# Kernel tuning notes

Measured on AMD Instinct MI355X. Metric: run time of the kernel, lower is better.

## Reference

```python
import jax, jax.numpy as jnp
import numpy as np

B, IN, H = 8192, 1024, 1024


def setup_inputs() -> dict:
    key = jax.random.key(0)
    kx, kh, kc, kwx, kwh = jax.random.split(key, 5)
    return {
        "x": jax.random.normal(kx, (B, IN), dtype=jnp.float32),
        "h": jax.random.normal(kh, (B, H), dtype=jnp.float32),
        "c": jax.random.normal(kc, (B, H), dtype=jnp.float32),
        # 8 Dense layers fused: gate order [i, f, g, o] along last axis
        "Wx": jax.random.normal(kwx, (IN, 4 * H), dtype=jnp.float32) * 0.02,
        "Wh": jax.random.normal(kwh, (H, 4 * H), dtype=jnp.float32) * 0.02,
        "bx": jnp.zeros((4 * H,), dtype=jnp.float32),
        "bh": jnp.zeros((4 * H,), dtype=jnp.float32),
    }


def reference(x, h, c, Wx, Wh, bx, bh):
    # Fused equivalent of the 8 separate Dense layers:
    #   gate_k = x @ Wx[:, k] + bx[k] + h @ Wh[:, k] + bh[k]
    gates = x @ Wx + h @ Wh + (bx + bh)  # [B, 4H]
    i, f, g, o = jnp.split(gates, 4, axis=-1)
    i = jax.nn.sigmoid(i)
    f = jax.nn.sigmoid(f)
    g = jnp.tanh(g)
    o = jax.nn.sigmoid(o)
    c_new = f * c + i * g
    h_new = o * jnp.tanh(c_new)
    # Original returns (out_gate, hidden_state, cell_state)
    return (o, h_new, c_new)
```

## Files before the change

### kernel.cpp

```cpp
#include <hip/hip_runtime.h>
#include <hip/hip_bf16.h>

typedef __attribute__((ext_vector_type(8))) short bf16x8;
typedef __attribute__((ext_vector_type(4))) float f32x4;
typedef __attribute__((ext_vector_type(4))) unsigned short u16x4;
typedef __attribute__((ext_vector_type(8))) unsigned short u16x8;

#define B_DIM 8192
#define H_DIM 1024
#define K_DIM 2048
#define N_DIM 4096
#define BH (B_DIM * H_DIM)

__device__ __forceinline__ unsigned short f2bf(float f) {
    union { float f; unsigned u; } v; v.f = f;
    unsigned r = v.u + 0x7FFFu + ((v.u >> 16) & 1u);
    return (unsigned short)(r >> 16);
}

__device__ __forceinline__ void gload16(const void* g, void* l) {
    __builtin_amdgcn_global_load_lds(
        (const __attribute__((address_space(1))) void*)g,
        (__attribute__((address_space(3))) void*)l, 16, 0, 0);
}

__global__ void build_a(const float* __restrict__ x, const float* __restrict__ h,
                        unsigned short* __restrict__ Abf) {
    int gid = blockIdx.x * 256 + threadIdx.x;
    int m   = gid >> 9;
    int rem = gid & 511;
    int p   = rem >> 8;
    int k4  = rem & 255;
    const float* src = (p ? h : x) + m * 1024 + k4 * 4;
    float4 v = *(const float4*)src;
    u16x4 o = { f2bf(v.x), f2bf(v.y), f2bf(v.z), f2bf(v.w) };
    *(u16x4*)(Abf + (size_t)gid * 4) = o;
}

__global__ void build_b(const float* __restrict__ Wx, const float* __restrict__ Wh,
                        unsigned short* __restrict__ Bperm) {
    __shared__ float tile[64][65];
    const int t  = threadIdx.x;
    const int k0 = blockIdx.x * 64;
    const int n0 = blockIdx.y * 64;
#pragma unroll
    for (int it = 0; it < 4; ++it) {
        int lin = it * 256 + t;
        int kl  = lin >> 4;
        int n4  = lin & 15;
        int k   = k0 + kl;
        const float* src = (k < 1024) ? (Wx + (size_t)k * 4096 + n0 + n4 * 4)
                                      : (Wh + (size_t)(k - 1024) * 4096 + n0 + n4 * 4);
        float4 v = *(const float4*)src;
        tile[kl][n4 * 4 + 0] = v.x;
        tile[kl][n4 * 4 + 1] = v.y;
        tile[kl][n4 * 4 + 2] = v.z;
        tile[kl][n4 * 4 + 3] = v.w;
    }
    __syncthreads();
#pragma unroll
    for (int it = 0; it < 2; ++it) {
        int lin = it * 256 + t;
        int nl  = lin >> 3;
        int ch  = lin & 7;
        int n    = n0 + nl;
        int gate = n >> 10;
        int j    = n & 1023;
        int jb   = j >> 5;
        int jj   = j & 31;
        int R    = jb * 128 + (jj >> 4) * 64 + gate * 16 + (jj & 15);
        u16x8 o;
#pragma unroll
        for (int q = 0; q < 8; ++q) o[q] = f2bf(tile[ch * 8 + q][nl]);
        *(u16x8*)(Bperm + (size_t)R * 2048 + k0 + ch * 8) = o;
    }
}

__global__ __launch_bounds__(256, 2) void lstm_fused(
    const unsigned short* __restrict__ Abf,
    const unsigned short* __restrict__ Bperm,
    const float* __restrict__ bx, const float* __restrict__ bh,
    const float* __restrict__ cin, float* __restrict__ out) {
    __shared__ unsigned short lsA[128 * 64];
    __shared__ unsigned short lsB[128 * 64];

    const int tid  = threadIdx.x;
    const int wave = tid >> 6;
    const int lane = tid & 63;
    const int m0 = blockIdx.x * 128;
    const int jb = blockIdx.y;
    const int wm = wave >> 1;
    const int wn = wave & 1;

    f32x4 acc[4][4];
#pragma unroll
    for (int i = 0; i < 4; ++i)
#pragma unroll
        for (int j = 0; j < 4; ++j) acc[i][j] = (f32x4){0.f, 0.f, 0.f, 0.f};

    const int sRow   = tid >> 3;
    const int sChunk = (tid & 7) * 8;
    const int aBase = (m0 + sRow) * K_DIM + sChunk;
    const int bBase = (jb * 128 + sRow) * K_DIM + sChunk;

    const int fRow = lane & 15;
    const int fK   = (lane >> 4) * 8;

    for (int kt = 0; kt < 32; ++kt) {
        const int kOff = kt * 64;
#pragma unroll
        for (int it = 0; it < 4; ++it) {
            gload16(Abf + aBase + it * (32 * K_DIM) + kOff, lsA + it * 2048 + wave * 512);
            gload16(Bperm + bBase + it * (32 * K_DIM) + kOff, lsB + it * 2048 + wave * 512);
        }
        __syncthreads();
#pragma unroll
        for (int ks = 0; ks < 2; ++ks) {
            bf16x8 af[4], bfr[4];
#pragma unroll
            for (int tm = 0; tm < 4; ++tm)
                af[tm] = *(const bf16x8*)(lsA + (wm * 64 + tm * 16 + fRow) * 64 + ks * 32 + fK);
#pragma unroll
            for (int tn = 0; tn < 4; ++tn)
                bfr[tn] = *(const bf16x8*)(lsB + (wn * 64 + tn * 16 + fRow) * 64 + ks * 32 + fK);
#pragma unroll
            for (int tm = 0; tm < 4; ++tm)
#pragma unroll
                for (int tn = 0; tn < 4; ++tn)
                    acc[tm][tn] = __builtin_amdgcn_mfma_f32_16x16x32_bf16(
                        af[tm], bfr[tn], acc[tm][tn], 0, 0, 0);
        }
        __syncthreads();
    }

    const int j = jb * 32 + wn * 16 + fRow;
    const float b_i = bx[j] + bh[j];
    const float b_f = bx[1024 + j] + bh[1024 + j];
    const float b_g = bx[2048 + j] + bh[2048 + j];
    const float b_o = bx[3072 + j] + bh[3072 + j];
#pragma unroll
    for (int tm = 0; tm < 4; ++tm) {
#pragma unroll
        for (int r = 0; r < 4; ++r) {
            const int row = m0 + wm * 64 + tm * 16 + (lane >> 4) * 4 + r;
            float vi = acc[tm][0][r] + b_i;
            float vf = acc[tm][1][r] + b_f;
            float vg = acc[tm][2][r] + b_g;
            float vo = acc[tm][3][r] + b_o;
            float ig = 1.f / (1.f + __expf(-vi));
            float fg = 1.f / (1.f + __expf(-vf));
            float e2g = __expf(2.f * fminf(fmaxf(vg, -15.f), 15.f));
            float gg = (e2g - 1.f) / (e2g + 1.f);
            float og = 1.f / (1.f + __expf(-vo));
            float cn = fg * cin[(size_t)row * 1024 + j] + ig * gg;
            float e2c = __expf(2.f * fminf(fmaxf(cn, -15.f), 15.f));
            float hn = og * ((e2c - 1.f) / (e2c + 1.f));
            out[(size_t)row * 1024 + j] = og;
            out[(size_t)BH + (size_t)row * 1024 + j] = hn;
            out[(size_t)2 * BH + (size_t)row * 1024 + j] = cn;
        }
    }
}

extern "C" void kernel_launch(void* const* d_in, const int* in_sizes, int n_in,
                              void* d_out, int out_size, void* d_ws, size_t ws_size,
                              hipStream_t stream) {
    const float* x  = (const float*)d_in[0];
    const float* h  = (const float*)d_in[1];
    const float* c  = (const float*)d_in[2];
    const float* Wx = (const float*)d_in[3];
    const float* Wh = (const float*)d_in[4];
    const float* bx = (const float*)d_in[5];
    const float* bh = (const float*)d_in[6];
    float* out = (float*)d_out;

    unsigned short* Abf   = (unsigned short*)d_ws;
    unsigned short* Bperm = (unsigned short*)((char*)d_ws + (size_t)B_DIM * K_DIM * 2);

    hipLaunchKernelGGL(build_a, dim3((B_DIM * K_DIM / 4) / 256), dim3(256), 0, stream, x, h, Abf);
    hipLaunchKernelGGL(build_b, dim3(32, 64), dim3(256), 0, stream, Wx, Wh, Bperm);
    hipLaunchKernelGGL(lstm_fused, dim3(B_DIM / 128, 32), dim3(256), 0, stream,
                       Abf, Bperm, bx, bh, c, out);
}
```

Baseline: 353.0 us.

## Swizzle LDS tiles, merge prep kernels, raise occupancy bound

Applies an XOR swizzle to the 16-byte chunk index in LDS for both A and B tiles, so the MFMA fragment reads no longer hit the same banks. Merges the two conversion kernels into one launch with 8-element vectorized A conversion. Raises the launch_bounds minimum to 4 blocks per SM, which caps registers per thread and risks spilling the 64 accumulators.

```diff
diff --git a/kernel.cpp b/kernel.cpp
--- a/kernel.cpp
+++ b/kernel.cpp
@@ -3,7 +3,6 @@
 
 typedef __attribute__((ext_vector_type(8))) short bf16x8;
 typedef __attribute__((ext_vector_type(4))) float f32x4;
-typedef __attribute__((ext_vector_type(4))) unsigned short u16x4;
 typedef __attribute__((ext_vector_type(8))) unsigned short u16x8;
 
 #define B_DIM 8192
@@ -24,25 +23,29 @@
         (__attribute__((address_space(3))) void*)l, 16, 0, 0);
 }
 
-__global__ void build_a(const float* __restrict__ x, const float* __restrict__ h,
-                        unsigned short* __restrict__ Abf) {
-    int gid = blockIdx.x * 256 + threadIdx.x;
-    int m   = gid >> 9;
-    int rem = gid & 511;
-    int p   = rem >> 8;
-    int k4  = rem & 255;
-    const float* src = (p ? h : x) + m * 1024 + k4 * 4;
-    float4 v = *(const float4*)src;
-    u16x4 o = { f2bf(v.x), f2bf(v.y), f2bf(v.z), f2bf(v.w) };
-    *(u16x4*)(Abf + (size_t)gid * 4) = o;
-}
-
-__global__ void build_b(const float* __restrict__ Wx, const float* __restrict__ Wh,
-                        unsigned short* __restrict__ Bperm) {
+__global__ void prep(const float* __restrict__ x, const float* __restrict__ h,
+                     const float* __restrict__ Wx, const float* __restrict__ Wh,
+                     unsigned short* __restrict__ Abf, unsigned short* __restrict__ Bperm) {
     __shared__ float tile[64][65];
-    const int t  = threadIdx.x;
-    const int k0 = blockIdx.x * 64;
-    const int n0 = blockIdx.y * 64;
+    const int t = threadIdx.x;
+    if (blockIdx.x < 8192) {
+        int gid = blockIdx.x * 256 + t;
+        size_t e = (size_t)gid * 8;
+        int m   = gid >> 8;
+        int col = (gid & 255) * 8;
+        int p   = col >> 10;
+        int k   = col & 1023;
+        const float* src = (p ? h : x) + (size_t)m * 1024 + k;
+        float4 v0 = *(const float4*)src;
+        float4 v1 = *(const float4*)(src + 4);
+        u16x8 o = { f2bf(v0.x), f2bf(v0.y), f2bf(v0.z), f2bf(v0.w),
+                    f2bf(v1.x), f2bf(v1.y), f2bf(v1.z), f2bf(v1.w) };
+        *(u16x8*)(Abf + e) = o;
+        return;
+    }
+    const int bz = blockIdx.x - 8192;
+    const int k0 = (bz & 31) * 64;
+    const int n0 = (bz >> 5) * 64;
 #pragma unroll
     for (int it = 0; it < 4; ++it) {
         int lin = it * 256 + t;
@@ -76,7 +79,7 @@
     }
 }
 
-__global__ __launch_bounds__(256, 2) void lstm_fused(
+__global__ __launch_bounds__(256, 4) void lstm_fused(
     const unsigned short* __restrict__ Abf,
     const unsigned short* __restrict__ Bperm,
     const float* __restrict__ bx, const float* __restrict__ bh,
@@ -99,12 +102,13 @@
         for (int j = 0; j < 4; ++j) acc[i][j] = (f32x4){0.f, 0.f, 0.f, 0.f};
 
     const int sRow   = tid >> 3;
-    const int sChunk = (tid & 7) * 8;
+    const int sChunk = (((tid & 7) ^ ((tid >> 3) & 7))) * 8;
     const int aBase = (m0 + sRow) * K_DIM + sChunk;
     const int bBase = (jb * 128 + sRow) * K_DIM + sChunk;
 
-    const int fRow = lane & 15;
-    const int fK   = (lane >> 4) * 8;
+    const int fRow  = lane & 15;
+    const int qBase = lane >> 4;
+    const int rx    = fRow & 7;
 
     for (int kt = 0; kt < 32; ++kt) {
         const int kOff = kt * 64;
@@ -117,12 +121,13 @@
 #pragma unroll
         for (int ks = 0; ks < 2; ++ks) {
             bf16x8 af[4], bfr[4];
+            const int qPhys = (ks * 4 + qBase) ^ rx;
 #pragma unroll
             for (int tm = 0; tm < 4; ++tm)
-                af[tm] = *(const bf16x8*)(lsA + (wm * 64 + tm * 16 + fRow) * 64 + ks * 32 + fK);
+                af[tm] = *(const bf16x8*)(lsA + (wm * 64 + tm * 16 + fRow) * 64 + qPhys * 8);
 #pragma unroll
             for (int tn = 0; tn < 4; ++tn)
-                bfr[tn] = *(const bf16x8*)(lsB + (wn * 64 + tn * 16 + fRow) * 64 + ks * 32 + fK);
+                bfr[tn] = *(const bf16x8*)(lsB + (wn * 64 + tn * 16 + fRow) * 64 + qPhys * 8);
 #pragma unroll
             for (int tm = 0; tm < 4; ++tm)
 #pragma unroll
@@ -177,8 +182,7 @@
     unsigned short* Abf   = (unsigned short*)d_ws;
     unsigned short* Bperm = (unsigned short*)((char*)d_ws + (size_t)B_DIM * K_DIM * 2);
 
-    hipLaunchKernelGGL(build_a, dim3((B_DIM * K_DIM / 4) / 256), dim3(256), 0, stream, x, h, Abf);
-    hipLaunchKernelGGL(build_b, dim3(32, 64), dim3(256), 0, stream, Wx, Wh, Bperm);
+    hipLaunchKernelGGL(prep, dim3(8192 + 2048), dim3(256), 0, stream, x, h, Wx, Wh, Abf, Bperm);
     hipLaunchKernelGGL(lstm_fused, dim3(B_DIM / 128, 32), dim3(256), 0, stream,
                        Abf, Bperm, bx, bh, c, out);
 }
```

Result: faster. 340.2 us (-3.6%).
